# Kernel tuning notes

Measured on AMD Instinct MI355X. Metric: run time of the kernel, lower is better.

Reference implementation:

```python
import jax, jax.numpy as jnp
import numpy as np

NUM_ITERATIONS = 3
EPS = 1e-7

def squash(v, axis=-1):
    # scale = |v|^2/(1+|v|^2) * v/sqrt(|v|^2+eps), matching the torch module
    sq = jnp.sum(v * v, axis=axis, keepdims=True)
    return (sq / (1.0 + sq)) * v / jnp.sqrt(sq + EPS)

def setup_inputs() -> dict:
    key = jax.random.key(0)
    kx, kw = jax.random.split(key)
    B, R, C, O, I = 256, 1152, 10, 16, 8
    x = jax.random.normal(kx, (B, R, I), dtype=jnp.float32)
    W = jax.random.normal(kw, (R, C, O, I), dtype=jnp.float32)
    return {"x": x, "W": W}

def reference(x, W):
    B, R, I = x.shape
    C, O = W.shape[1], W.shape[2]
    # u_hat[b,r,c,o] = sum_i W[r,c,o,i] * x[b,r,i]  (batched tiny GEMV)
    u_hat = jnp.einsum('rcoi,bri->brco', W, x)
    b_ij = jnp.zeros((B, R, C), dtype=u_hat.dtype)
    v = None
    for it in range(NUM_ITERATIONS):
        c_ij = jax.nn.softmax(b_ij, axis=1)          # softmax over route nodes (dim=1, as in source)
        s_j = jnp.einsum('brc,brco->bco', c_ij, u_hat)
        v = squash(s_j, axis=-1)                      # squash over out_channels (dim=-2 of the 5D torch tensor)
        if it != NUM_ITERATIONS - 1:
            b_ij = b_ij + jnp.einsum('brco,bco->brc', u_hat, v)
    # match torch output shape (B, 1, C, O, 1)
    return v[:, None, :, :, None]
```

## Files before the change

kernel.cpp:

```cpp
#include <hip/hip_runtime.h>
#include <cstdint>

#define BB 256
#define RR 1152
#define CC 10
#define OO 16
#define II 8
#define NT 768
#define GG 2
#define NWAVE (NT / 64)
#define PSTR 1189

__device__ __forceinline__ void unpack2(uint32_t pk, float& lo, float& hi) {
    union { uint32_t i; float f; } a, b;
    a.i = pk << 16; b.i = pk & 0xffff0000u;
    lo = a.f; hi = b.f;
}
__device__ __forceinline__ float dot4(float4 a, float4 b) {
    float s = a.x * b.x;
    s = fmaf(a.y, b.y, s); s = fmaf(a.z, b.z, s); s = fmaf(a.w, b.w, s);
    return s;
}
__device__ __forceinline__ float qpadd1(float v) {
    int o = __builtin_amdgcn_mov_dpp(__float_as_int(v), 0xB1, 0xF, 0xF, true);
    return v + __int_as_float(o);
}
__device__ __forceinline__ float qpadd2(float v) {
    int o = __builtin_amdgcn_mov_dpp(__float_as_int(v), 0x4E, 0xF, 0xF, true);
    return v + __int_as_float(o);
}
__device__ __forceinline__ float dppx2f(float v) {
    return __int_as_float(__builtin_amdgcn_mov_dpp(__float_as_int(v), 0x4E, 0xF, 0xF, true));
}
__device__ __forceinline__ uint32_t cvtpk(float lo, float hi) {
    uint32_t r;
    asm("v_cvt_pk_bf16_f32 %0, %1, %2" : "=v"(r) : "v"(lo), "v"(hi));
    return r;
}

__global__ __launch_bounds__(NT, 6)
void k_caps(const float* __restrict__ x, const float* __restrict__ W,
            float* __restrict__ out) {
    extern __shared__ uint32_t u2[];
    __shared__ float part[NWAVE][17];
    __shared__ float p0s[NWAVE][8][4][GG];
    __shared__ float wsum[GG][OO];

    const int t = threadIdx.x;
    const int c  = blockIdx.x / (BB / GG);
    const int b0 = (blockIdx.x % (BB / GG)) * GG;
    const int wv = t >> 6, l = t & 63;
    const int rg = t >> 3, p = t & 7;

    uint32_t* uA = u2;
    uint32_t* uB = u2 + 8 * PSTR;

    const int pw = 2 * (p & 3) + (p >> 2);
    uint32_t* wrA = uA + pw * PSTR;
    uint32_t* wrB = uB + pw * PSTR;

    float s00 = 0.f, s01 = 0.f, s02 = 0.f, s03 = 0.f;
    float s10 = 0.f, s11 = 0.f, s12 = 0.f, s13 = 0.f;
#pragma unroll 2
    for (int it = 0; it < RR / 96; ++it) {
        const int r = it * 96 + rg;
        const float* wrow = W + ((size_t)r * CC + c) * (OO * II) + p * 4;
        float4 w0 = *reinterpret_cast<const float4*>(wrow);
        float4 w1 = *reinterpret_cast<const float4*>(wrow + 32);
        float4 w2 = *reinterpret_cast<const float4*>(wrow + 64);
        float4 w3 = *reinterpret_cast<const float4*>(wrow + 96);
        const float* xp = x + ((size_t)b0 * RR + r) * II + (p & 1) * 4;
        float4 xh0 = *reinterpret_cast<const float4*>(xp);
        float4 xh1 = *reinterpret_cast<const float4*>(xp + (size_t)RR * II);

        float d0 = qpadd1(dot4(w0, xh0));
        float d1 = qpadd1(dot4(w1, xh0));
        float d2 = qpadd1(dot4(w2, xh0));
        float d3 = qpadd1(dot4(w3, xh0));
        s00 += d0; s01 += d1; s02 += d2; s03 += d3;
        {
            uint32_t q0 = cvtpk(d0, dppx2f(d0));
            uint32_t q1 = cvtpk(d1, dppx2f(d1));
            uint32_t q2 = cvtpk(d2, dppx2f(d2));
            uint32_t q3 = cvtpk(d3, dppx2f(d3));
            uint32_t sa = (p & 2) ? ((p & 1) ? q3 : q2) : ((p & 1) ? q1 : q0);
            wrA[r] = sa;
        }
        float e0 = qpadd1(dot4(w0, xh1));
        float e1 = qpadd1(dot4(w1, xh1));
        float e2 = qpadd1(dot4(w2, xh1));
        float e3 = qpadd1(dot4(w3, xh1));
        s10 += e0; s11 += e1; s12 += e2; s13 += e3;
        {
            uint32_t q0 = cvtpk(e0, dppx2f(e0));
            uint32_t q1 = cvtpk(e1, dppx2f(e1));
            uint32_t q2 = cvtpk(e2, dppx2f(e2));
            uint32_t q3 = cvtpk(e3, dppx2f(e3));
            uint32_t sa = (p & 2) ? ((p & 1) ? q3 : q2) : ((p & 1) ? q1 : q0);
            wrB[r] = sa;
        }
    }
#pragma unroll
    for (int m = 8; m < 64; m <<= 1) {
        s00 += __shfl_xor(s00, m); s01 += __shfl_xor(s01, m);
        s02 += __shfl_xor(s02, m); s03 += __shfl_xor(s03, m);
        s10 += __shfl_xor(s10, m); s11 += __shfl_xor(s11, m);
        s12 += __shfl_xor(s12, m); s13 += __shfl_xor(s13, m);
    }
    if (l < 8) {
        p0s[wv][l][0][0] = s00; p0s[wv][l][1][0] = s01;
        p0s[wv][l][2][0] = s02; p0s[wv][l][3][0] = s03;
        p0s[wv][l][0][1] = s10; p0s[wv][l][1][1] = s11;
        p0s[wv][l][2][1] = s12; p0s[wv][l][3][1] = s13;
    }
    __syncthreads();

    if (t < GG * OO) {
        const int g = t >> 4, o = t & 15;
        float s = 0.f;
#pragma unroll
        for (int w = 0; w < NWAVE; ++w) s += p0s[w][2 * (o & 3)][o >> 2][g];
        s *= (1.0f / RR);
        float ss = s * s;
        ss += __shfl_xor(ss, 1); ss += __shfl_xor(ss, 2);
        ss += __shfl_xor(ss, 4); ss += __shfl_xor(ss, 8);
        wsum[g][o] = s * (ss / ((1.0f + ss) * sqrtf(ss + 1e-7f)));
    }
    __syncthreads();

    const int g2 = wv / 6;
    const int wv6 = wv - g2 * 6;
    const uint32_t* ug = g2 ? uB : uA;
    const int q = l & 3;
    const int rl = l >> 2;
    const uint32_t* rp0 = ug + (size_t)q * PSTR;
    const uint32_t* rp1 = ug + (size_t)(q + 4) * PSTR;
    const int rbase = wv6 * 16 + rl;

    for (int pass = 1; pass < 3; ++pass) {
        const float wq0 = wsum[g2][2 * q];
        const float wq1 = wsum[g2][2 * q + 1];
        const float wq2 = wsum[g2][2 * q + 8];
        const float wq3 = wsum[g2][2 * q + 9];
        float n0 = 0.f, n1 = 0.f, n2 = 0.f, n3 = 0.f, den = 0.f;

#pragma unroll
        for (int it2 = 0; it2 < 12; ++it2) {
            const int r = it2 * 96 + rbase;
            uint32_t pa = rp0[r];
            uint32_t pb = rp1[r];
            float u0, u1, u2, u3;
            unpack2(pa, u0, u1);
            unpack2(pb, u3, u2);
            float lg = fmaf(u1, wq1, u0 * wq0);
            lg = fmaf(u2, wq2, lg);
            lg = fmaf(u3, wq3, lg);
            lg = qpadd1(lg);
            lg = qpadd2(lg);
            float e = __expf(lg);
            den += e;
            n0 = fmaf(e, u0, n0); n1 = fmaf(e, u1, n1);
            n2 = fmaf(e, u2, n2); n3 = fmaf(e, u3, n3);
        }

#pragma unroll
        for (int m = 4; m < 64; m <<= 1) {
            n0 += __shfl_xor(n0, m); n1 += __shfl_xor(n1, m);
            n2 += __shfl_xor(n2, m); n3 += __shfl_xor(n3, m);
            den += __shfl_xor(den, m);
        }
        if (l < 4) {
            part[wv][2 * l]     = n0;
            part[wv][2 * l + 1] = n1;
            part[wv][2 * l + 8] = n2;
            part[wv][2 * l + 9] = n3;
            if (l == 0) part[wv][16] = den;
        }
        __syncthreads();

        if (t < GG * OO) {
            const int g = t >> 4, o = t & 15;
            float nf = 0.f, df = 0.f;
#pragma unroll
            for (int w = 0; w < 6; ++w) {
                nf += part[6 * g + w][o];
                df += part[6 * g + w][16];
            }
            float s = nf / df;
            float ss = s * s;
            ss += __shfl_xor(ss, 1); ss += __shfl_xor(ss, 2);
            ss += __shfl_xor(ss, 4); ss += __shfl_xor(ss, 8);
            float v = s * (ss / ((1.0f + ss) * sqrtf(ss + 1e-7f)));
            if (pass == 2)
                out[((size_t)(b0 + g) * CC + c) * OO + o] = v;
            else
                wsum[g][o] += v;
        }
        __syncthreads();
    }
}

extern "C" void kernel_launch(void* const* d_in, const int* in_sizes, int n_in,
                              void* d_out, int out_size, void* d_ws, size_t ws_size,
                              hipStream_t stream) {
    const float* x = (const float*)d_in[0];
    const float* W = (const float*)d_in[1];
    if (n_in >= 2 && in_sizes[0] == RR * CC * OO * II &&
        in_sizes[1] == BB * RR * II) {
        const float* tmp = x; x = W; W = tmp;
    }
    float* out = (float*)d_out;

    const size_t dyn_lds = (size_t)GG * 8 * PSTR * 4;
    k_caps<<<CC * (BB / GG), NT, dyn_lds, stream>>>(x, W, out);
}
```

Measured before the change: 109.7 us.

## Interleave bf16 u_hat LDS layout per route row and use packed float2 math

Switches the shared-memory u_hat store from eight padded planes (one per packed output pair) to a row-interleaved layout holding eight packed words per route node. Each routing lane can then fetch its two words with a single 64-bit LDS load instead of two scalar loads. The logit and weighted-sum arithmetic is rewritten with two-wide float vectors so the compiler can emit packed FMA instructions. The tradeoff is that the padding stride is removed, which may bring back LDS bank conflicts on the write side, and the LDS footprint shrinks slightly.

```diff
diff --git a/kernel.cpp b/kernel.cpp
--- a/kernel.cpp
+++ b/kernel.cpp
@@ -9,12 +9,14 @@
 #define NT 768
 #define GG 2
 #define NWAVE (NT / 64)
-#define PSTR 1189
-
-__device__ __forceinline__ void unpack2(uint32_t pk, float& lo, float& hi) {
-    union { uint32_t i; float f; } a, b;
-    a.i = pk << 16; b.i = pk & 0xffff0000u;
-    lo = a.f; hi = b.f;
+
+typedef float float2v __attribute__((ext_vector_type(2)));
+
+__device__ __forceinline__ float bflo(uint32_t pk) {
+    union { uint32_t i; float f; } a; a.i = pk << 16; return a.f;
+}
+__device__ __forceinline__ float bfhi(uint32_t pk) {
+    union { uint32_t i; float f; } a; a.i = pk & 0xffff0000u; return a.f;
 }
 __device__ __forceinline__ float dot4(float4 a, float4 b) {
     float s = a.x * b.x;
@@ -53,11 +55,11 @@
     const int rg = t >> 3, p = t & 7;
 
     uint32_t* uA = u2;
-    uint32_t* uB = u2 + 8 * PSTR;
-
-    const int pw = 2 * (p & 3) + (p >> 2);
-    uint32_t* wrA = uA + pw * PSTR;
-    uint32_t* wrB = uB + pw * PSTR;
+    uint32_t* uB = u2 + (size_t)RR * 8;
+
+    const int pos = (p >> 1) + ((p & 1) << 2);
+    uint32_t* wrA = uA + (size_t)rg * 8 + pos;
+    uint32_t* wrB = uB + (size_t)rg * 8 + pos;
 
     float s00 = 0.f, s01 = 0.f, s02 = 0.f, s03 = 0.f;
     float s10 = 0.f, s11 = 0.f, s12 = 0.f, s13 = 0.f;
@@ -84,7 +86,7 @@
             uint32_t q2 = cvtpk(d2, dppx2f(d2));
             uint32_t q3 = cvtpk(d3, dppx2f(d3));
             uint32_t sa = (p & 2) ? ((p & 1) ? q3 : q2) : ((p & 1) ? q1 : q0);
-            wrA[r] = sa;
+            wrA[(size_t)it * 768] = sa;
         }
         float e0 = qpadd1(dot4(w0, xh1));
         float e1 = qpadd1(dot4(w1, xh1));
@@ -97,7 +99,7 @@
             uint32_t q2 = cvtpk(e2, dppx2f(e2));
             uint32_t q3 = cvtpk(e3, dppx2f(e3));
             uint32_t sa = (p & 2) ? ((p & 1) ? q3 : q2) : ((p & 1) ? q1 : q0);
-            wrB[r] = sa;
+            wrB[(size_t)it * 768] = sa;
         }
     }
 #pragma unroll
@@ -133,36 +135,32 @@
     const uint32_t* ug = g2 ? uB : uA;
     const int q = l & 3;
     const int rl = l >> 2;
-    const uint32_t* rp0 = ug + (size_t)q * PSTR;
-    const uint32_t* rp1 = ug + (size_t)(q + 4) * PSTR;
     const int rbase = wv6 * 16 + rl;
+    const uint32_t* rp = ug + (size_t)rbase * 8 + 2 * q;
 
     for (int pass = 1; pass < 3; ++pass) {
-        const float wq0 = wsum[g2][2 * q];
-        const float wq1 = wsum[g2][2 * q + 1];
-        const float wq2 = wsum[g2][2 * q + 8];
-        const float wq3 = wsum[g2][2 * q + 9];
-        float n0 = 0.f, n1 = 0.f, n2 = 0.f, n3 = 0.f, den = 0.f;
+        const float2v WQA = { wsum[g2][2 * q],     wsum[g2][2 * q + 8] };
+        const float2v WQB = { wsum[g2][2 * q + 1], wsum[g2][2 * q + 9] };
+        float2v N0 = { 0.f, 0.f }, N1 = { 0.f, 0.f };
+        float den = 0.f;
 
 #pragma unroll
         for (int it2 = 0; it2 < 12; ++it2) {
-            const int r = it2 * 96 + rbase;
-            uint32_t pa = rp0[r];
-            uint32_t pb = rp1[r];
-            float u0, u1, u2, u3;
-            unpack2(pa, u0, u1);
-            unpack2(pb, u3, u2);
-            float lg = fmaf(u1, wq1, u0 * wq0);
-            lg = fmaf(u2, wq2, lg);
-            lg = fmaf(u3, wq3, lg);
+            uint2 pp = *reinterpret_cast<const uint2*>(rp + (size_t)it2 * 768);
+            float2v P0 = { bflo(pp.x), bfhi(pp.y) };
+            float2v P1 = { bfhi(pp.x), bflo(pp.y) };
+            float2v lg2 = __builtin_elementwise_fma(P0, WQA, P1 * WQB);
+            float lg = lg2.x + lg2.y;
             lg = qpadd1(lg);
             lg = qpadd2(lg);
             float e = __expf(lg);
             den += e;
-            n0 = fmaf(e, u0, n0); n1 = fmaf(e, u1, n1);
-            n2 = fmaf(e, u2, n2); n3 = fmaf(e, u3, n3);
-        }
-
+            float2v E2 = { e, e };
+            N0 = __builtin_elementwise_fma(E2, P0, N0);
+            N1 = __builtin_elementwise_fma(E2, P1, N1);
+        }
+
+        float n0 = N0.x, n2 = N0.y, n1 = N1.x, n3 = N1.y;
 #pragma unroll
         for (int m = 4; m < 64; m <<= 1) {
             n0 += __shfl_xor(n0, m); n1 += __shfl_xor(n1, m);
@@ -211,6 +209,6 @@
     }
     float* out = (float*)d_out;
 
-    const size_t dyn_lds = (size_t)GG * 8 * PSTR * 4;
+    const size_t dyn_lds = (size_t)GG * RR * 8 * 4;
     k_caps<<<CC * (BB / GG), NT, dyn_lds, stream>>>(x, W, out);
 }
```

Result: no change. 107.9 us (-1.6%).
